# Performance work log

Measured on AMD Instinct MI355X. Metric: run time of the kernel, lower is better.

The kernel has to match this reference:

```python
import jax, jax.numpy as jnp
import numpy as np

ALPHA = 0.2  # LeakyReLU negative slope
NEG_BIG = jnp.float32(-9e15)


def _leaky_relu(x):
    return jnp.where(x > 0, x, ALPHA * x)


def gat_layer(h, adj, w, a):
    """One GATLayer with concat=True (ELU output), dropout=0 (eval mode).
    h: [N, F_in], adj: [N, N] int, w: [F_in, F_out], a: [2*F_out, 1].
    """
    Wh = h @ w                         # [N, F_out]
    f_out = w.shape[1]
    Wh1 = Wh @ a[:f_out]               # [N, 1]
    Wh2 = Wh @ a[f_out:]               # [N, 1]
    e = _leaky_relu(Wh1 + Wh2.T)       # [N, N] dense additive scores
    att = jnp.where(adj > 0, e, NEG_BIG)
    att = jax.nn.softmax(att, axis=1)  # row softmax
    return jax.nn.elu(att @ Wh)        # [N, F_out]


def setup_inputs() -> dict:
    N, F_IN, H, NHEADS = 4096, 128, 64, 4
    key = jax.random.key(0)
    ks = jax.random.split(key, 9)
    s = jnp.float32(0.1)  # keep logits in a sane range
    x = jax.random.normal(ks[0], (N, F_IN), jnp.float32)
    adj = jax.random.randint(ks[1], (N, N), 0, 2, jnp.int32)
    return {
        "x": x,
        "adj": adj,
        "w_heads": jax.random.normal(ks[2], (NHEADS, F_IN, H), jnp.float32) * s,
        "a_heads": jax.random.normal(ks[3], (NHEADS, 2 * H, 1), jnp.float32) * s,
        "w_out": jax.random.normal(ks[4], (NHEADS * H, H), jnp.float32) * s,
        "a_out": jax.random.normal(ks[5], (2 * H, 1), jnp.float32) * s,
        "lin_w": jax.random.normal(ks[6], (H, F_IN), jnp.float32) * s,
        "lin_b": jnp.zeros((H,), jnp.float32),
        "outlin_w": jax.random.normal(ks[7], (H, H), jnp.float32) * s,
        "outlin_b": jnp.zeros((H,), jnp.float32),
    }


def reference(x, adj, w_heads, a_heads, w_out, a_out, lin_w, lin_b, outlin_w, outlin_b):
    N = x.shape[0]
    x_residual = x @ lin_w.T + lin_b                      # nn.Linear(input, hidden)
    # multi-head GAT layers, concatenated along features
    heads = jax.vmap(gat_layer, in_axes=(None, None, 0, 0))(x, adj, w_heads, a_heads)  # [nh, N, H]
    hcat = jnp.transpose(heads, (1, 0, 2)).reshape(N, -1)  # [N, nh*H]
    out = gat_layer(hcat, adj, w_out, a_out)               # out_att (concat=True => ELU)
    out = (x_residual + out) @ outlin_w.T + outlin_b       # out_linear
    return jax.nn.elu(out)
```

## Files before the change

### kernel.cpp

```cpp
#include <hip/hip_runtime.h>
#include <hip/hip_bf16.h>
#include <stdint.h>

#define F_IN 128
#define H 64
#define NH 4
#define KCH_H 8
#define KCH_O 16
#define LOG2E 1.44269504088896f

typedef __attribute__((ext_vector_type(8))) short bf16x8;
typedef __attribute__((ext_vector_type(4))) float floatx4;

__global__ void pack_adjp_kernel(const int4* __restrict__ adj4,
                                 unsigned char* __restrict__ adjp,
                                 int N, int KT) {
    int row = blockIdx.y;
    int c0 = (blockIdx.x * 256 + threadIdx.x) * 8;
    const int4* p = adj4 + ((size_t)row * N + c0) / 4;
    int4 a = p[0], b = p[1];
    unsigned int byte =
        (unsigned)(a.x > 0) | ((unsigned)(a.y > 0) << 1) |
        ((unsigned)(a.z > 0) << 2) | ((unsigned)(a.w > 0) << 3) |
        ((unsigned)(b.x > 0) << 4) | ((unsigned)(b.y > 0) << 5) |
        ((unsigned)(b.z > 0) << 6) | ((unsigned)(b.w > 0) << 7);
    int kt = c0 >> 5, q = (c0 >> 3) & 3;
    adjp[((size_t)(row >> 4) * KT + kt) * 64 + q * 16 + (row & 15)] =
        (unsigned char)byte;
}

__global__ void wh_fused_kernel(const float* __restrict__ x,
                                const float* __restrict__ w_heads,
                                const float* __restrict__ a_heads,
                                const float* __restrict__ lin_w,
                                const float* __restrict__ lin_b,
                                float* __restrict__ Wh_all,
                                float* __restrict__ x_res,
                                float* __restrict__ s1h,
                                float* __restrict__ s2h, int N) {
    int tid = threadIdx.x;
    int h = tid >> 6, f = tid & 63;
    int i0 = blockIdx.x * 8;
    __shared__ float xs[8][F_IN];
    for (int e = tid; e < 8 * F_IN; e += 256)
        xs[e >> 7][e & 127] = x[(size_t)(i0 + (e >> 7)) * F_IN + (e & 127)];
    __syncthreads();
    float acc[8];
#pragma unroll
    for (int r = 0; r < 8; ++r) acc[r] = 0.f;
    float xr0 = 0.f, xr1 = 0.f;
    const float* w = w_heads + (size_t)h * F_IN * H + f;
    const float* lw = lin_w + (size_t)f * F_IN;
#pragma unroll 4
    for (int k = 0; k < F_IN; ++k) {
        float wv = w[(size_t)k * H];
#pragma unroll
        for (int r = 0; r < 8; ++r) acc[r] += xs[r][k] * wv;
        float wx = lw[k];
        xr0 += xs[h][k] * wx;
        xr1 += xs[h + 4][k] * wx;
    }
#pragma unroll
    for (int r = 0; r < 8; ++r)
        Wh_all[((size_t)h * N + i0 + r) * H + f] = acc[r];
    float b = lin_b[f];
    x_res[(size_t)(i0 + h) * H + f] = xr0 + b;
    x_res[(size_t)(i0 + h + 4) * H + f] = xr1 + b;
    float a1v = a_heads[(size_t)h * 2 * H + f];
    float a2v = a_heads[(size_t)h * 2 * H + H + f];
#pragma unroll
    for (int r = 0; r < 8; ++r) {
        float t1 = acc[r] * a1v;
        float t2 = acc[r] * a2v;
#pragma unroll
        for (int off = 32; off > 0; off >>= 1) {
            t1 += __shfl_xor(t1, off, 64);
            t2 += __shfl_xor(t2, off, 64);
        }
        if (f == 0) {
            s1h[(size_t)h * N + i0 + r] = t1 * LOG2E;
            s2h[(size_t)h * N + i0 + r] = t2 * LOG2E;
        }
    }
}

__global__ void bpack_kernel(const float* __restrict__ src,
                             unsigned short* __restrict__ dst, int N) {
    int h = blockIdx.y, kt = blockIdx.x;
    int KT = N >> 5;
    int tid = threadIdx.x;
    int g = tid >> 6, lane = tid & 63;
    int q = lane >> 4, n = lane & 15;
    const float* s = src + ((size_t)h * N + kt * 32 + q * 8) * 64 + g * 16 + n;
    unsigned short tmp[8];
#pragma unroll
    for (int jj = 0; jj < 8; ++jj) {
        __hip_bfloat16 b = __float2bfloat16(s[(size_t)jj * 64]);
        tmp[jj] = *(unsigned short*)&b;
    }
    unsigned short* d = dst + (((size_t)(h * KT + kt) * 4 + g) * 64 + lane) * 8;
#pragma unroll
    for (int jj = 0; jj < 8; ++jj) d[jj] = tmp[jj];
}

template <int KTC>
__global__ __launch_bounds__(256, 8)
void pv2_kernel(const unsigned char* __restrict__ adjp,
                const unsigned short* __restrict__ Bpk,
                const float* __restrict__ s1a,
                const float* __restrict__ s2a,
                float* __restrict__ outp, float* __restrict__ lp,
                int out_stride, int N) {
    const int h = blockIdx.y, z = blockIdx.z;
    const int KT = N >> 5;
    const int kt0 = z * KTC;
    const int tid = threadIdx.x;
    const int wave = tid >> 6, lane = tid & 63;
    const int n = lane & 15, q = lane >> 4;
    const int i0w = (blockIdx.x * 4 + wave) * 16;

    __shared__ float s2s[KTC * 32];
    __shared__ unsigned short ldsB[2][2048];

    const float4* s2src = (const float4*)(s2a + (size_t)h * N + kt0 * 32);
    for (int e = tid; e < KTC * 8; e += 256) ((float4*)s2s)[e] = s2src[e];

    const unsigned short* Bb = Bpk + ((size_t)h * KT + kt0) * 2048;
    *(uint4*)&ldsB[0][tid * 8] = *(const uint4*)(Bb + tid * 8);

    const unsigned char* ap = adjp + ((size_t)(i0w >> 4) * KT + kt0) * 64 + lane;
    unsigned int a_c = ap[0];
    const float s1v = s1a[(size_t)h * N + i0w + n];

    floatx4 acc[4];
    floatx4 accl = {0.f, 0.f, 0.f, 0.f};
#pragma unroll
    for (int g = 0; g < 4; ++g) acc[g] = (floatx4){0.f, 0.f, 0.f, 0.f};

    bf16x8 ones;
    {
        short one = (n == 0) ? (short)0x3F80 : (short)0;
#pragma unroll
        for (int jj = 0; jj < 8; ++jj) ones[jj] = one;
    }

    __syncthreads();

#pragma unroll 2
    for (int k = 0; k < KTC; ++k) {
        const int cur = k & 1;
        const int kn = (k + 1 < KTC) ? k + 1 : k;
        uint4 bst = *(const uint4*)(Bb + (size_t)kn * 2048 + tid * 8);
        unsigned int a_n = ap[(size_t)kn * 64];

        float4 sa = *(const float4*)&s2s[k * 32 + q * 8];
        float4 sb = *(const float4*)&s2s[k * 32 + q * 8 + 4];
        const float* sv = (const float*)&sa;
        const float* sw = (const float*)&sb;
        float e[8];
#pragma unroll
        for (int jj = 0; jj < 8; ++jj) {
            float sj = (jj < 4 ? sv[jj] : sw[jj - 4]);
            float tt = s1v + sj;
            float lr = fmaxf(tt, 0.2f * tt);
            lr = (a_c & (1u << jj)) ? lr : -150.f;
            e[jj] = __builtin_amdgcn_exp2f(lr);
        }
        union { unsigned int u[4]; bf16x8 v; } u;
        u.u[0] = __builtin_amdgcn_perm(__float_as_uint(e[1]), __float_as_uint(e[0]), 0x07060302u);
        u.u[1] = __builtin_amdgcn_perm(__float_as_uint(e[3]), __float_as_uint(e[2]), 0x07060302u);
        u.u[2] = __builtin_amdgcn_perm(__float_as_uint(e[5]), __float_as_uint(e[4]), 0x07060302u);
        u.u[3] = __builtin_amdgcn_perm(__float_as_uint(e[7]), __float_as_uint(e[6]), 0x07060302u);

        bf16x8 bf0 = *(const bf16x8*)&ldsB[cur][0 * 512 + lane * 8];
        bf16x8 bf1 = *(const bf16x8*)&ldsB[cur][1 * 512 + lane * 8];
        bf16x8 bf2 = *(const bf16x8*)&ldsB[cur][2 * 512 + lane * 8];
        bf16x8 bf3 = *(const bf16x8*)&ldsB[cur][3 * 512 + lane * 8];

        acc[0] = __builtin_amdgcn_mfma_f32_16x16x32_bf16(u.v, bf0, acc[0], 0, 0, 0);
        acc[1] = __builtin_amdgcn_mfma_f32_16x16x32_bf16(u.v, bf1, acc[1], 0, 0, 0);
        acc[2] = __builtin_amdgcn_mfma_f32_16x16x32_bf16(u.v, bf2, acc[2], 0, 0, 0);
        acc[3] = __builtin_amdgcn_mfma_f32_16x16x32_bf16(u.v, bf3, acc[3], 0, 0, 0);
        accl   = __builtin_amdgcn_mfma_f32_16x16x32_bf16(u.v, ones, accl, 0, 0, 0);

        *(uint4*)&ldsB[cur ^ 1][tid * 8] = bst;
        a_c = a_n;
        __syncthreads();
    }

    float* obase = outp + ((size_t)z * N + i0w) * out_stride + h * 64;
#pragma unroll
    for (int r = 0; r < 4; ++r) {
        int rr = q * 4 + r;
        float* op = obase + (size_t)rr * out_stride + n;
        op[0]  = acc[0][r];
        op[16] = acc[1][r];
        op[32] = acc[2][r];
        op[48] = acc[3][r];
    }
    if (n == 0) {
        float* lrow = lp + ((size_t)z * gridDim.y + h) * N + i0w;
#pragma unroll
        for (int r = 0; r < 4; ++r) lrow[q * 4 + r] = accl[r];
    }
}

__global__ void whout2_kernel(const float* __restrict__ hcp,
                              const float* __restrict__ lhp,
                              const float* __restrict__ w_out,
                              const float* __restrict__ a_out,
                              float* __restrict__ Wh_out,
                              float* __restrict__ s1o,
                              float* __restrict__ s2o, int N) {
    int tid = threadIdx.x;
    int i0 = blockIdx.x * 8;
    __shared__ float hs[8][256];
    __shared__ float linv[8][NH];
    if (tid < 8 * NH) {
        int r = tid >> 2, hd = tid & 3;
        float l = 0.f;
#pragma unroll
        for (int p = 0; p < KCH_H; ++p)
            l += lhp[((size_t)p * NH + hd) * N + i0 + r];
        linv[r][hd] = 1.f / fmaxf(l, 1e-30f);
    }
    __syncthreads();
    const size_t ps = (size_t)N * 256;
    for (int e = tid; e < 8 * 256; e += 256) {
        int r = e >> 8, k = e & 255;
        size_t off = (size_t)(i0 + r) * 256 + k;
        float v = 0.f;
#pragma unroll
        for (int p = 0; p < KCH_H; ++p) v += hcp[p * ps + off];
        v *= linv[r][k >> 6];
        hs[r][k] = v > 0.f ? v : expm1f(v);
    }
    __syncthreads();
    int f = tid & 63, rl = tid >> 6;
    float a0 = 0.f, a1 = 0.f;
#pragma unroll 4
    for (int k = 0; k < 256; ++k) {
        float wv = w_out[(size_t)k * H + f];
        a0 += hs[rl][k] * wv;
        a1 += hs[rl + 4][k] * wv;
    }
    Wh_out[(size_t)(i0 + rl) * H + f] = a0;
    Wh_out[(size_t)(i0 + rl + 4) * H + f] = a1;
    float w1 = a_out[f], w2 = a_out[H + f];
    float t10 = a0 * w1, t20 = a0 * w2, t11 = a1 * w1, t21 = a1 * w2;
#pragma unroll
    for (int off = 32; off > 0; off >>= 1) {
        t10 += __shfl_xor(t10, off, 64);
        t20 += __shfl_xor(t20, off, 64);
        t11 += __shfl_xor(t11, off, 64);
        t21 += __shfl_xor(t21, off, 64);
    }
    if (f == 0) {
        s1o[i0 + rl] = t10 * LOG2E;
        s2o[i0 + rl] = t20 * LOG2E;
        s1o[i0 + rl + 4] = t11 * LOG2E;
        s2o[i0 + rl + 4] = t21 * LOG2E;
    }
}

__global__ void final2_kernel(const float* __restrict__ o2p,
                              const float* __restrict__ lop,
                              const float* __restrict__ x_res,
                              const float* __restrict__ outlin_w,
                              const float* __restrict__ outlin_b,
                              float* __restrict__ out, int N) {
    int tid = threadIdx.x;
    int f = tid & 63, rl = tid >> 6;
    int i0 = blockIdx.x * 8;
    __shared__ float hs[8][H];
    __shared__ float linv[8];
    if (tid < 8) {
        float l = 0.f;
#pragma unroll
        for (int p = 0; p < KCH_O; ++p) l += lop[(size_t)p * N + i0 + tid];
        linv[tid] = 1.f / fmaxf(l, 1e-30f);
    }
    __syncthreads();
    const size_t ps = (size_t)N * 64;
    for (int e = tid; e < 8 * 64; e += 256) {
        int r = e >> 6, ff = e & 63;
        size_t off = (size_t)(i0 + r) * 64 + ff;
        float v = 0.f;
#pragma unroll
        for (int p = 0; p < KCH_O; ++p) v += o2p[p * ps + off];
        v *= linv[r];
        v = v > 0.f ? v : expm1f(v);
        hs[r][ff] = v + x_res[off];
    }
    __syncthreads();
    float b = outlin_b[f];
    float a0 = b, a1 = b;
#pragma unroll 8
    for (int k = 0; k < H; ++k) {
        float wv = outlin_w[(size_t)f * H + k];
        a0 += hs[rl][k] * wv;
        a1 += hs[rl + 4][k] * wv;
    }
    a0 = a0 > 0.f ? a0 : expm1f(a0);
    a1 = a1 > 0.f ? a1 : expm1f(a1);
    out[(size_t)(i0 + rl) * H + f] = a0;
    out[(size_t)(i0 + rl + 4) * H + f] = a1;
}

extern "C" void kernel_launch(void* const* d_in, const int* in_sizes, int n_in,
                              void* d_out, int out_size, void* d_ws, size_t ws_size,
                              hipStream_t stream) {
    const float* x        = (const float*)d_in[0];
    const int*   adj      = (const int*)d_in[1];
    const float* w_heads  = (const float*)d_in[2];
    const float* a_heads  = (const float*)d_in[3];
    const float* w_out    = (const float*)d_in[4];
    const float* a_out    = (const float*)d_in[5];
    const float* lin_w    = (const float*)d_in[6];
    const float* lin_b    = (const float*)d_in[7];
    const float* outlin_w = (const float*)d_in[8];
    const float* outlin_b = (const float*)d_in[9];
    float* out = (float*)d_out;

    const int N = in_sizes[0] / F_IN;
    const int KT = N >> 5;

    char* p = (char*)d_ws;
    float* part   = (float*)p;  p += (size_t)KCH_H * N * 256 * 4;
    float* Wh_all = (float*)p;  p += (size_t)NH * N * 64 * 4;
    float* x_res  = (float*)p;  p += (size_t)N * 64 * 4;
    float* Wh_out = (float*)p;  p += (size_t)N * 64 * 4;
    float* s1h    = (float*)p;  p += (size_t)NH * N * 4;
    float* s2h    = (float*)p;  p += (size_t)NH * N * 4;
    float* s1o    = (float*)p;  p += (size_t)N * 4;
    float* s2o    = (float*)p;  p += (size_t)N * 4;
    float* lh_part = (float*)p; p += (size_t)KCH_H * NH * N * 4;
    float* lo_part = (float*)p; p += (size_t)KCH_O * N * 4;
    unsigned short* Bpk  = (unsigned short*)p;  p += (size_t)NH * KT * 2048 * 2;
    unsigned short* BpkO = (unsigned short*)p;  p += (size_t)KT * 2048 * 2;
    unsigned char* adjp  = (unsigned char*)p;   p += (size_t)(N / 16) * KT * 64;

    pack_adjp_kernel<<<dim3(N / 2048, N), 256, 0, stream>>>((const int4*)adj, adjp, N, KT);
    wh_fused_kernel<<<N / 8, 256, 0, stream>>>(x, w_heads, a_heads, lin_w, lin_b,
                                               Wh_all, x_res, s1h, s2h, N);
    bpack_kernel<<<dim3(KT, NH), 256, 0, stream>>>(Wh_all, Bpk, N);

    pv2_kernel<16><<<dim3(N / 64, NH, KCH_H), 256, 0, stream>>>(
        adjp, Bpk, s1h, s2h, part, lh_part, NH * H, N);
    whout2_kernel<<<N / 8, 256, 0, stream>>>(part, lh_part, w_out, a_out,
                                             Wh_out, s1o, s2o, N);
    bpack_kernel<<<dim3(KT, 1), 256, 0, stream>>>(Wh_out, BpkO, N);
    pv2_kernel<8><<<dim3(N / 64, 1, KCH_O), 256, 0, stream>>>(
        adjp, BpkO, s1o, s2o, part, lo_part, H, N);
    final2_kernel<<<N / 8, 256, 0, stream>>>(part, lo_part, x_res, outlin_w, outlin_b, out, N);
}
```

Measured before the change: 206.0 us.

## Fuse bf16 B-packing into producers and use double-buffered 32-row PV kernel for heads

Removes both bpack kernels by having wh_fused_kernel and whout2_kernel write the bf16 MFMA-packed B layout directly, which drops the fp32 Wh intermediates and two launches. Adds a new pv3 kernel for the head layer in which each wave handles 32 rows (two 16-row tiles), so every B fragment staged in LDS feeds twice as many MFMAs. That kernel double-buffers B through LDS, prefetching the next tile into registers during the current compute step. The trade-off is higher register use, with launch bounds lowered to 4 blocks, and half as many blocks in the grid.

Result: slower. 211.0 us (+2.4%).

```diff
diff --git a/kernel.cpp b/kernel.cpp
--- a/kernel.cpp
+++ b/kernel.cpp
@@ -11,6 +11,11 @@
 
 typedef __attribute__((ext_vector_type(8))) short bf16x8;
 typedef __attribute__((ext_vector_type(4))) float floatx4;
+
+static __device__ __forceinline__ unsigned short f2bf(float v) {
+    __hip_bfloat16 b = __float2bfloat16(v);
+    return *(unsigned short*)&b;
+}
 
 __global__ void pack_adjp_kernel(const int4* __restrict__ adj4,
                                  unsigned char* __restrict__ adjp,
@@ -34,13 +39,14 @@
                                 const float* __restrict__ a_heads,
                                 const float* __restrict__ lin_w,
                                 const float* __restrict__ lin_b,
-                                float* __restrict__ Wh_all,
+                                unsigned short* __restrict__ Bpk,
                                 float* __restrict__ x_res,
                                 float* __restrict__ s1h,
                                 float* __restrict__ s2h, int N) {
     int tid = threadIdx.x;
     int h = tid >> 6, f = tid & 63;
     int i0 = blockIdx.x * 8;
+    int KT = N >> 5;
     __shared__ float xs[8][F_IN];
     for (int e = tid; e < 8 * F_IN; e += 256)
         xs[e >> 7][e & 127] = x[(size_t)(i0 + (e >> 7)) * F_IN + (e & 127)];
@@ -60,9 +66,15 @@
         xr0 += xs[h][k] * wx;
         xr1 += xs[h + 4][k] * wx;
     }
-#pragma unroll
-    for (int r = 0; r < 8; ++r)
-        Wh_all[((size_t)h * N + i0 + r) * H + f] = acc[r];
+    {
+        int kt = i0 >> 5, qq = (i0 >> 3) & 3;
+        union { unsigned short s[8]; uint4 v; } t;
+#pragma unroll
+        for (int r = 0; r < 8; ++r) t.s[r] = f2bf(acc[r]);
+        unsigned short* d = Bpk +
+            (((size_t)(h * KT + kt) * 4 + (f >> 4)) * 64 + qq * 16 + (f & 15)) * 8;
+        *(uint4*)d = t.v;
+    }
     float b = lin_b[f];
     x_res[(size_t)(i0 + h) * H + f] = xr0 + b;
     x_res[(size_t)(i0 + h + 4) * H + f] = xr1 + b;
@@ -84,23 +96,122 @@
     }
 }
 
-__global__ void bpack_kernel(const float* __restrict__ src,
-                             unsigned short* __restrict__ dst, int N) {
-    int h = blockIdx.y, kt = blockIdx.x;
-    int KT = N >> 5;
-    int tid = threadIdx.x;
-    int g = tid >> 6, lane = tid & 63;
-    int q = lane >> 4, n = lane & 15;
-    const float* s = src + ((size_t)h * N + kt * 32 + q * 8) * 64 + g * 16 + n;
-    unsigned short tmp[8];
-#pragma unroll
-    for (int jj = 0; jj < 8; ++jj) {
-        __hip_bfloat16 b = __float2bfloat16(s[(size_t)jj * 64]);
-        tmp[jj] = *(unsigned short*)&b;
-    }
-    unsigned short* d = dst + (((size_t)(h * KT + kt) * 4 + g) * 64 + lane) * 8;
-#pragma unroll
-    for (int jj = 0; jj < 8; ++jj) d[jj] = tmp[jj];
+template <int KTC>
+__global__ __launch_bounds__(256, 4)
+void pv3_kernel(const unsigned char* __restrict__ adjp,
+                const unsigned short* __restrict__ Bpk,
+                const float* __restrict__ s1a,
+                const float* __restrict__ s2a,
+                float* __restrict__ outp, float* __restrict__ lp,
+                int out_stride, int N) {
+    const int h = blockIdx.y, z = blockIdx.z;
+    const int KT = N >> 5;
+    const int kt0 = z * KTC;
+    const int tid = threadIdx.x;
+    const int wave = tid >> 6, lane = tid & 63;
+    const int n = lane & 15, q = lane >> 4;
+    const int i0w = (blockIdx.x * 4 + wave) * 32;
+
+    __shared__ float s2s[KTC * 32];
+    __shared__ unsigned short ldsB[2][2048];
+
+    const float4* s2src = (const float4*)(s2a + (size_t)h * N + kt0 * 32);
+    for (int e = tid; e < KTC * 8; e += 256) ((float4*)s2s)[e] = s2src[e];
+
+    const unsigned short* Bb = Bpk + ((size_t)h * KT + kt0) * 2048;
+    *(uint4*)&ldsB[0][tid * 8] = *(const uint4*)(Bb + tid * 8);
+
+    const unsigned char* arow0 = adjp + ((size_t)(i0w >> 4) * KT + kt0) * 64 + lane;
+    const unsigned char* arow1 = arow0 + (size_t)KT * 64;
+    unsigned int a_c0 = arow0[0], a_c1 = arow1[0];
+    const float s1v0 = s1a[(size_t)h * N + i0w + n];
+    const float s1v1 = s1a[(size_t)h * N + i0w + 16 + n];
+
+    floatx4 acc[2][4];
+    floatx4 accl[2];
+#pragma unroll
+    for (int t = 0; t < 2; ++t) {
+        accl[t] = (floatx4){0.f, 0.f, 0.f, 0.f};
+#pragma unroll
+        for (int g = 0; g < 4; ++g) acc[t][g] = (floatx4){0.f, 0.f, 0.f, 0.f};
+    }
+
+    bf16x8 ones;
+    {
+        short one = (n == 0) ? (short)0x3F80 : (short)0;
+#pragma unroll
+        for (int jj = 0; jj < 8; ++jj) ones[jj] = one;
+    }
+
+    __syncthreads();
+
+    for (int k = 0; k < KTC; ++k) {
+        const int cur = k & 1;
+        const int kn = (k + 1 < KTC) ? k + 1 : k;
+        uint4 bst = *(const uint4*)(Bb + (size_t)kn * 2048 + tid * 8);
+        unsigned int a_n0 = arow0[(size_t)kn * 64];
+        unsigned int a_n1 = arow1[(size_t)kn * 64];
+
+        float4 sa = *(const float4*)&s2s[k * 32 + q * 8];
+        float4 sb = *(const float4*)&s2s[k * 32 + q * 8 + 4];
+        const float* sv = (const float*)&sa;
+        const float* sw = (const float*)&sb;
+
+        bf16x8 af[2];
+#pragma unroll
+        for (int t = 0; t < 2; ++t) {
+            const float s1v = t ? s1v1 : s1v0;
+            const unsigned int ab = t ? a_c1 : a_c0;
+            float e[8];
+#pragma unroll
+            for (int jj = 0; jj < 8; ++jj) {
+                float sj = (jj < 4 ? sv[jj] : sw[jj - 4]);
+                float tt = s1v + sj;
+                float lr = fmaxf(tt, 0.2f * tt);
+                lr = (ab & (1u << jj)) ? lr : -150.f;
+                e[jj] = __builtin_amdgcn_exp2f(lr);
+            }
+            union { unsigned int u[4]; bf16x8 v; } u;
+            u.u[0] = __builtin_amdgcn_perm(__float_as_uint(e[1]), __float_as_uint(e[0]), 0x07060302u);
+            u.u[1] = __builtin_amdgcn_perm(__float_as_uint(e[3]), __float_as_uint(e[2]), 0x07060302u);
+            u.u[2] = __builtin_amdgcn_perm(__float_as_uint(e[5]), __float_as_uint(e[4]), 0x07060302u);
+            u.u[3] = __builtin_amdgcn_perm(__float_as_uint(e[7]), __float_as_uint(e[6]), 0x07060302u);
+            af[t] = u.v;
+        }
+
+#pragma unroll
+        for (int g = 0; g < 4; ++g) {
+            bf16x8 bf = *(const bf16x8*)&ldsB[cur][g * 512 + lane * 8];
+            acc[0][g] = __builtin_amdgcn_mfma_f32_16x16x32_bf16(af[0], bf, acc[0][g], 0, 0, 0);
+            acc[1][g] = __builtin_amdgcn_mfma_f32_16x16x32_bf16(af[1], bf, acc[1][g], 0, 0, 0);
+        }
+        accl[0] = __builtin_amdgcn_mfma_f32_16x16x32_bf16(af[0], ones, accl[0], 0, 0, 0);
+        accl[1] = __builtin_amdgcn_mfma_f32_16x16x32_bf16(af[1], ones, accl[1], 0, 0, 0);
+
+        *(uint4*)&ldsB[cur ^ 1][tid * 8] = bst;
+        a_c0 = a_n0;
+        a_c1 = a_n1;
+        __syncthreads();
+    }
+
+#pragma unroll
+    for (int t = 0; t < 2; ++t) {
+        float* obase = outp + ((size_t)z * N + i0w + t * 16) * out_stride + h * 64;
+#pragma unroll
+        for (int r = 0; r < 4; ++r) {
+            int rr = q * 4 + r;
+            float* op = obase + (size_t)rr * out_stride + n;
+            op[0]  = acc[t][0][r];
+            op[16] = acc[t][1][r];
+            op[32] = acc[t][2][r];
+            op[48] = acc[t][3][r];
+        }
+        if (n == 0) {
+            float* lrow = lp + ((size_t)z * gridDim.y + h) * N + i0w + t * 16;
+#pragma unroll
+            for (int r = 0; r < 4; ++r) lrow[q * 4 + r] = accl[t][r];
+        }
+    }
 }
 
 template <int KTC>
@@ -209,11 +320,12 @@
                               const float* __restrict__ lhp,
                               const float* __restrict__ w_out,
                               const float* __restrict__ a_out,
-                              float* __restrict__ Wh_out,
+                              unsigned short* __restrict__ BpkO,
                               float* __restrict__ s1o,
                               float* __restrict__ s2o, int N) {
     int tid = threadIdx.x;
     int i0 = blockIdx.x * 8;
+    int KT = N >> 5;
     __shared__ float hs[8][256];
     __shared__ float linv[8][NH];
     if (tid < 8 * NH) {
@@ -244,8 +356,6 @@
         a0 += hs[rl][k] * wv;
         a1 += hs[rl + 4][k] * wv;
     }
-    Wh_out[(size_t)(i0 + rl) * H + f] = a0;
-    Wh_out[(size_t)(i0 + rl + 4) * H + f] = a1;
     float w1 = a_out[f], w2 = a_out[H + f];
     float t10 = a0 * w1, t20 = a0 * w2, t11 = a1 * w1, t21 = a1 * w2;
 #pragma unroll
@@ -260,6 +370,21 @@
         s2o[i0 + rl] = t20 * LOG2E;
         s1o[i0 + rl + 4] = t11 * LOG2E;
         s2o[i0 + rl + 4] = t21 * LOG2E;
+    }
+    __syncthreads();
+    float* wsW = &hs[0][0];
+    wsW[rl * 64 + f] = a0;
+    wsW[(rl + 4) * 64 + f] = a1;
+    __syncthreads();
+    if (tid < 64) {
+        int kt = i0 >> 5, qq = (i0 >> 3) & 3;
+        int g = tid >> 4, n = tid & 15;
+        union { unsigned short s[8]; uint4 v; } t;
+#pragma unroll
+        for (int r = 0; r < 8; ++r) t.s[r] = f2bf(wsW[r * 64 + g * 16 + n]);
+        unsigned short* d = BpkO +
+            (((size_t)kt * 4 + g) * 64 + qq * 16 + n) * 8;
+        *(uint4*)d = t.v;
     }
 }
 
@@ -327,9 +452,7 @@
 
     char* p = (char*)d_ws;
     float* part   = (float*)p;  p += (size_t)KCH_H * N * 256 * 4;
-    float* Wh_all = (float*)p;  p += (size_t)NH * N * 64 * 4;
     float* x_res  = (float*)p;  p += (size_t)N * 64 * 4;
-    float* Wh_out = (float*)p;  p += (size_t)N * 64 * 4;
     float* s1h    = (float*)p;  p += (size_t)NH * N * 4;
     float* s2h    = (float*)p;  p += (size_t)NH * N * 4;
     float* s1o    = (float*)p;  p += (size_t)N * 4;
@@ -342,14 +465,11 @@
 
     pack_adjp_kernel<<<dim3(N / 2048, N), 256, 0, stream>>>((const int4*)adj, adjp, N, KT);
     wh_fused_kernel<<<N / 8, 256, 0, stream>>>(x, w_heads, a_heads, lin_w, lin_b,
-                                               Wh_all, x_res, s1h, s2h, N);
-    bpack_kernel<<<dim3(KT, NH), 256, 0, stream>>>(Wh_all, Bpk, N);
-
-    pv2_kernel<16><<<dim3(N / 64, NH, KCH_H), 256, 0, stream>>>(
+                                               Bpk, x_res, s1h, s2h, N);
+    pv3_kernel<16><<<dim3(N / 128, NH, KCH_H), 256, 0, stream>>>(
         adjp, Bpk, s1h, s2h, part, lh_part, NH * H, N);
     whout2_kernel<<<N / 8, 256, 0, stream>>>(part, lh_part, w_out, a_out,
-                                             Wh_out, s1o, s2o, N);
-    bpack_kernel<<<dim3(KT, 1), 256, 0, stream>>>(Wh_out, BpkO, N);
+                                             BpkO, s1o, s2o, N);
     pv2_kernel<8><<<dim3(N / 64, 1, KCH_O), 256, 0, stream>>>(
         adjp, BpkO, s1o, s2o, part, lo_part, H, N);
     final2_kernel<<<N / 8, 256, 0, stream>>>(part, lo_part, x_res, outlin_w, outlin_b, out, N);
```

## Fuse adjacency packing, Wh projection and bf16 B-packing into fewer kernels

Applied to the files above, without the earlier changes.

Merges the adjacency bit-packing and the per-head Wh projection into one prep kernel, dispatched by block index. It writes Wh straight into the bf16 MFMA B-tile layout, so the float Wh buffers and both bpack kernels are no longer needed. whout2 likewise packs its output into BpkO through shared memory. The pv2 loop is also reworked to prefetch B tiles and adjacency bytes two steps ahead, with the LDS store moved to the top of the iteration. This removes three launches and the fp32 round trips, at the cost of a more complex prefetch schedule and more register pressure.

Result: slower. 228.4 us (+10.9%).

```diff
diff --git a/kernel.cpp b/kernel.cpp
--- a/kernel.cpp
+++ b/kernel.cpp
@@ -12,35 +12,43 @@
 typedef __attribute__((ext_vector_type(8))) short bf16x8;
 typedef __attribute__((ext_vector_type(4))) float floatx4;
 
-__global__ void pack_adjp_kernel(const int4* __restrict__ adj4,
-                                 unsigned char* __restrict__ adjp,
-                                 int N, int KT) {
-    int row = blockIdx.y;
-    int c0 = (blockIdx.x * 256 + threadIdx.x) * 8;
-    const int4* p = adj4 + ((size_t)row * N + c0) / 4;
-    int4 a = p[0], b = p[1];
-    unsigned int byte =
-        (unsigned)(a.x > 0) | ((unsigned)(a.y > 0) << 1) |
-        ((unsigned)(a.z > 0) << 2) | ((unsigned)(a.w > 0) << 3) |
-        ((unsigned)(b.x > 0) << 4) | ((unsigned)(b.y > 0) << 5) |
-        ((unsigned)(b.z > 0) << 6) | ((unsigned)(b.w > 0) << 7);
-    int kt = c0 >> 5, q = (c0 >> 3) & 3;
-    adjp[((size_t)(row >> 4) * KT + kt) * 64 + q * 16 + (row & 15)] =
-        (unsigned char)byte;
-}
-
-__global__ void wh_fused_kernel(const float* __restrict__ x,
-                                const float* __restrict__ w_heads,
-                                const float* __restrict__ a_heads,
-                                const float* __restrict__ lin_w,
-                                const float* __restrict__ lin_b,
-                                float* __restrict__ Wh_all,
-                                float* __restrict__ x_res,
-                                float* __restrict__ s1h,
-                                float* __restrict__ s2h, int N) {
+static __device__ __forceinline__ unsigned short f2bf(float v) {
+    __hip_bfloat16 b = __float2bfloat16(v);
+    return *(unsigned short*)&b;
+}
+
+__global__ void prep_kernel(const int4* __restrict__ adj4,
+                            unsigned char* __restrict__ adjp,
+                            const float* __restrict__ x,
+                            const float* __restrict__ w_heads,
+                            const float* __restrict__ a_heads,
+                            const float* __restrict__ lin_w,
+                            const float* __restrict__ lin_b,
+                            unsigned short* __restrict__ Bpk,
+                            float* __restrict__ x_res,
+                            float* __restrict__ s1h,
+                            float* __restrict__ s2h, int N) {
+    int bid = blockIdx.x;
     int tid = threadIdx.x;
+    int KT = N >> 5;
+    if (bid < 2 * N) {
+        int row = bid >> 1;
+        int c0 = ((bid & 1) * 256 + tid) * 8;
+        const int4* p = adj4 + ((size_t)row * N + c0) / 4;
+        int4 a = p[0], b = p[1];
+        unsigned int byte =
+            (unsigned)(a.x > 0) | ((unsigned)(a.y > 0) << 1) |
+            ((unsigned)(a.z > 0) << 2) | ((unsigned)(a.w > 0) << 3) |
+            ((unsigned)(b.x > 0) << 4) | ((unsigned)(b.y > 0) << 5) |
+            ((unsigned)(b.z > 0) << 6) | ((unsigned)(b.w > 0) << 7);
+        int kt = c0 >> 5, q = (c0 >> 3) & 3;
+        adjp[((size_t)(row >> 4) * KT + kt) * 64 + q * 16 + (row & 15)] =
+            (unsigned char)byte;
+        return;
+    }
+    int blk = bid - 2 * N;
     int h = tid >> 6, f = tid & 63;
-    int i0 = blockIdx.x * 8;
+    int i0 = blk * 8;
     __shared__ float xs[8][F_IN];
     for (int e = tid; e < 8 * F_IN; e += 256)
         xs[e >> 7][e & 127] = x[(size_t)(i0 + (e >> 7)) * F_IN + (e & 127)];
@@ -60,9 +68,15 @@
         xr0 += xs[h][k] * wx;
         xr1 += xs[h + 4][k] * wx;
     }
-#pragma unroll
-    for (int r = 0; r < 8; ++r)
-        Wh_all[((size_t)h * N + i0 + r) * H + f] = acc[r];
+    {
+        int kt = i0 >> 5, qq = (i0 >> 3) & 3;
+        union { unsigned short s[8]; uint4 v; } t;
+#pragma unroll
+        for (int r = 0; r < 8; ++r) t.s[r] = f2bf(acc[r]);
+        unsigned short* d = Bpk +
+            (((size_t)(h * KT + kt) * 4 + (f >> 4)) * 64 + qq * 16 + (f & 15)) * 8;
+        *(uint4*)d = t.v;
+    }
     float b = lin_b[f];
     x_res[(size_t)(i0 + h) * H + f] = xr0 + b;
     x_res[(size_t)(i0 + h + 4) * H + f] = xr1 + b;
@@ -82,25 +96,6 @@
             s2h[(size_t)h * N + i0 + r] = t2 * LOG2E;
         }
     }
-}
-
-__global__ void bpack_kernel(const float* __restrict__ src,
-                             unsigned short* __restrict__ dst, int N) {
-    int h = blockIdx.y, kt = blockIdx.x;
-    int KT = N >> 5;
-    int tid = threadIdx.x;
-    int g = tid >> 6, lane = tid & 63;
-    int q = lane >> 4, n = lane & 15;
-    const float* s = src + ((size_t)h * N + kt * 32 + q * 8) * 64 + g * 16 + n;
-    unsigned short tmp[8];
-#pragma unroll
-    for (int jj = 0; jj < 8; ++jj) {
-        __hip_bfloat16 b = __float2bfloat16(s[(size_t)jj * 64]);
-        tmp[jj] = *(unsigned short*)&b;
-    }
-    unsigned short* d = dst + (((size_t)(h * KT + kt) * 4 + g) * 64 + lane) * 8;
-#pragma unroll
-    for (int jj = 0; jj < 8; ++jj) d[jj] = tmp[jj];
 }
 
 template <int KTC>
@@ -126,10 +121,13 @@
     for (int e = tid; e < KTC * 8; e += 256) ((float4*)s2s)[e] = s2src[e];
 
     const unsigned short* Bb = Bpk + ((size_t)h * KT + kt0) * 2048;
-    *(uint4*)&ldsB[0][tid * 8] = *(const uint4*)(Bb + tid * 8);
+    uint4 breg = *(const uint4*)(Bb + tid * 8);
+    *(uint4*)&ldsB[0][tid * 8] = breg;
+    breg = *(const uint4*)(Bb + 2048 + tid * 8);
 
     const unsigned char* ap = adjp + ((size_t)(i0w >> 4) * KT + kt0) * 64 + lane;
     unsigned int a_c = ap[0];
+    unsigned int a_n = ap[64];
     const float s1v = s1a[(size_t)h * N + i0w + n];
 
     floatx4 acc[4];
@@ -148,10 +146,12 @@
 
 #pragma unroll 2
     for (int k = 0; k < KTC; ++k) {
-        const int cur = k & 1;
-        const int kn = (k + 1 < KTC) ? k + 1 : k;
-        uint4 bst = *(const uint4*)(Bb + (size_t)kn * 2048 + tid * 8);
-        unsigned int a_n = ap[(size_t)kn * 64];
+        if (k + 1 < KTC) *(uint4*)&ldsB[(k + 1) & 1][tid * 8] = breg;
+        unsigned int a_2 = 0;
+        if (k + 2 < KTC) {
+            breg = *(const uint4*)(Bb + (size_t)(k + 2) * 2048 + tid * 8);
+            a_2 = ap[(size_t)(k + 2) * 64];
+        }
 
         float4 sa = *(const float4*)&s2s[k * 32 + q * 8];
         float4 sb = *(const float4*)&s2s[k * 32 + q * 8 + 4];
@@ -172,10 +172,10 @@
         u.u[2] = __builtin_amdgcn_perm(__float_as_uint(e[5]), __float_as_uint(e[4]), 0x07060302u);
         u.u[3] = __builtin_amdgcn_perm(__float_as_uint(e[7]), __float_as_uint(e[6]), 0x07060302u);
 
-        bf16x8 bf0 = *(const bf16x8*)&ldsB[cur][0 * 512 + lane * 8];
-        bf16x8 bf1 = *(const bf16x8*)&ldsB[cur][1 * 512 + lane * 8];
-        bf16x8 bf2 = *(const bf16x8*)&ldsB[cur][2 * 512 + lane * 8];
-        bf16x8 bf3 = *(const bf16x8*)&ldsB[cur][3 * 512 + lane * 8];
+        bf16x8 bf0 = *(const bf16x8*)&ldsB[k & 1][0 * 512 + lane * 8];
+        bf16x8 bf1 = *(const bf16x8*)&ldsB[k & 1][1 * 512 + lane * 8];
+        bf16x8 bf2 = *(const bf16x8*)&ldsB[k & 1][2 * 512 + lane * 8];
+        bf16x8 bf3 = *(const bf16x8*)&ldsB[k & 1][3 * 512 + lane * 8];
 
         acc[0] = __builtin_amdgcn_mfma_f32_16x16x32_bf16(u.v, bf0, acc[0], 0, 0, 0);
         acc[1] = __builtin_amdgcn_mfma_f32_16x16x32_bf16(u.v, bf1, acc[1], 0, 0, 0);
@@ -183,8 +183,8 @@
         acc[3] = __builtin_amdgcn_mfma_f32_16x16x32_bf16(u.v, bf3, acc[3], 0, 0, 0);
         accl   = __builtin_amdgcn_mfma_f32_16x16x32_bf16(u.v, ones, accl, 0, 0, 0);
 
-        *(uint4*)&ldsB[cur ^ 1][tid * 8] = bst;
         a_c = a_n;
+        a_n = a_2;
         __syncthreads();
     }
 
@@ -209,11 +209,12 @@
                               const float* __restrict__ lhp,
                               const float* __restrict__ w_out,
                               const float* __restrict__ a_out,
-                              float* __restrict__ Wh_out,
+                              unsigned short* __restrict__ BpkO,
                               float* __restrict__ s1o,
                               float* __restrict__ s2o, int N) {
     int tid = threadIdx.x;
     int i0 = blockIdx.x * 8;
+    int KT = N >> 5;
     __shared__ float hs[8][256];
     __shared__ float linv[8][NH];
     if (tid < 8 * NH) {
@@ -244,8 +245,6 @@
         a0 += hs[rl][k] * wv;
         a1 += hs[rl + 4][k] * wv;
     }
-    Wh_out[(size_t)(i0 + rl) * H + f] = a0;
-    Wh_out[(size_t)(i0 + rl + 4) * H + f] = a1;
     float w1 = a_out[f], w2 = a_out[H + f];
     float t10 = a0 * w1, t20 = a0 * w2, t11 = a1 * w1, t21 = a1 * w2;
 #pragma unroll
@@ -260,6 +259,21 @@
         s2o[i0 + rl] = t20 * LOG2E;
         s1o[i0 + rl + 4] = t11 * LOG2E;
         s2o[i0 + rl + 4] = t21 * LOG2E;
+    }
+    __syncthreads();
+    float* wsW = &hs[0][0];
+    wsW[rl * 64 + f] = a0;
+    wsW[(rl + 4) * 64 + f] = a1;
+    __syncthreads();
+    if (tid < 64) {
+        int kt = i0 >> 5, qq = (i0 >> 3) & 3;
+        int g = tid >> 4, nn = tid & 15;
+        union { unsigned short s[8]; uint4 v; } t;
+#pragma unroll
+        for (int r = 0; r < 8; ++r) t.s[r] = f2bf(wsW[r * 64 + g * 16 + nn]);
+        unsigned short* d = BpkO +
+            (((size_t)kt * 4 + g) * 64 + qq * 16 + nn) * 8;
+        *(uint4*)d = t.v;
     }
 }
 
@@ -327,9 +341,7 @@
 
     char* p = (char*)d_ws;
     float* part   = (float*)p;  p += (size_t)KCH_H * N * 256 * 4;
-    float* Wh_all = (float*)p;  p += (size_t)NH * N * 64 * 4;
     float* x_res  = (float*)p;  p += (size_t)N * 64 * 4;
-    float* Wh_out = (float*)p;  p += (size_t)N * 64 * 4;
     float* s1h    = (float*)p;  p += (size_t)NH * N * 4;
     float* s2h    = (float*)p;  p += (size_t)NH * N * 4;
     float* s1o    = (float*)p;  p += (size_t)N * 4;
@@ -340,16 +352,13 @@
     unsigned short* BpkO = (unsigned short*)p;  p += (size_t)KT * 2048 * 2;
     unsigned char* adjp  = (unsigned char*)p;   p += (size_t)(N / 16) * KT * 64;
 
-    pack_adjp_kernel<<<dim3(N / 2048, N), 256, 0, stream>>>((const int4*)adj, adjp, N, KT);
-    wh_fused_kernel<<<N / 8, 256, 0, stream>>>(x, w_heads, a_heads, lin_w, lin_b,
-                                               Wh_all, x_res, s1h, s2h, N);
-    bpack_kernel<<<dim3(KT, NH), 256, 0, stream>>>(Wh_all, Bpk, N);
-
+    prep_kernel<<<2 * N + N / 8, 256, 0, stream>>>(
+        (const int4*)adj, adjp, x, w_heads, a_heads, lin_w, lin_b,
+        Bpk, x_res, s1h, s2h, N);
     pv2_kernel<16><<<dim3(N / 64, NH, KCH_H), 256, 0, stream>>>(
         adjp, Bpk, s1h, s2h, part, lh_part, NH * H, N);
     whout2_kernel<<<N / 8, 256, 0, stream>>>(part, lh_part, w_out, a_out,
-                                             Wh_out, s1o, s2o, N);
-    bpack_kernel<<<dim3(KT, 1), 256, 0, stream>>>(Wh_out, BpkO, N);
+                                             BpkO, s1o, s2o, N);
     pv2_kernel<8><<<dim3(N / 64, 1, KCH_O), 256, 0, stream>>>(
         adjp, BpkO, s1o, s2o, part, lo_part, H, N);
     final2_kernel<<<N / 8, 256, 0, stream>>>(part, lo_part, x_res, outlin_w, outlin_b, out, N);
```
